# Performance work log

Measured on AMD Instinct MI355X. Metric: run time of the kernel, lower is better.

## Reference

```python
import jax, jax.numpy as jnp
import numpy as np

N_EMBD = 1024
N_HEAD = 16
HEAD_DIM = N_EMBD // N_HEAD
INNER = 4 * N_EMBD
EPS = 1e-5


def setup_inputs() -> dict:
    key = jax.random.key(0)
    ks = jax.random.split(key, 13)
    s = lambda d: 1.0 / np.sqrt(d)
    return {
        "x": jax.random.normal(ks[0], (2, 2048, N_EMBD), jnp.float32),
        "ln1_g": jnp.ones((N_EMBD,), jnp.float32),
        "ln1_b": jnp.zeros((N_EMBD,), jnp.float32),
        "w_attn": jax.random.normal(ks[1], (N_EMBD, 3 * N_EMBD), jnp.float32) * s(N_EMBD),
        "b_attn": jnp.zeros((3 * N_EMBD,), jnp.float32),
        "w_proj": jax.random.normal(ks[2], (N_EMBD, N_EMBD), jnp.float32) * s(N_EMBD),
        "b_proj": jnp.zeros((N_EMBD,), jnp.float32),
        "ln2_g": jnp.ones((N_EMBD,), jnp.float32),
        "ln2_b": jnp.zeros((N_EMBD,), jnp.float32),
        "w_fc": jax.random.normal(ks[3], (N_EMBD, INNER), jnp.float32) * s(N_EMBD),
        "b_fc": jnp.zeros((INNER,), jnp.float32),
        "w_fc2": jax.random.normal(ks[4], (INNER, N_EMBD), jnp.float32) * s(INNER),
        "b_fc2": jnpp if False else jnp.zeros((N_EMBD,), jnp.float32),
    }


def _layernorm(x, g, b):
    mu = jnp.mean(x, axis=-1, keepdims=True)
    var = jnp.mean(jnp.square(x - mu), axis=-1, keepdims=True)
    return (x - mu) * jax.lax.rsqrt(var + EPS) * g + b


def _attention(x, w_attn, b_attn, w_proj, b_proj):
    B, T, C = x.shape
    qkv = x @ w_attn + b_attn                      # [B,T,3C]
    q, k, v = jnp.split(qkv, 3, axis=-1)
    q = q.reshape(B, T, N_HEAD, HEAD_DIM).transpose(0, 2, 1, 3)  # [B,H,T,D]
    k = k.reshape(B, T, N_HEAD, HEAD_DIM).transpose(0, 2, 1, 3)
    v = v.reshape(B, T, N_HEAD, HEAD_DIM).transpose(0, 2, 1, 3)
    scale = HEAD_DIM ** -0.5
    scores = jnp.einsum("bhqd,bhkd->bhqk", q, k) * scale         # [B,H,T,T]
    causal = jnp.triu(jnp.ones((T, T), jnp.bool_), k=1)
    scores = jnp.where(causal, -jnp.inf, scores)
    attn = jax.nn.softmax(scores, axis=-1)
    out = jnp.einsum("bhqk,bhkd->bhqd", attn, v)                 # [B,H,T,D]
    out = out.transpose(0, 2, 1, 3).reshape(B, T, C)
    return out @ w_proj + b_proj


def reference(x, ln1_g, ln1_b, w_attn, b_attn, w_proj, b_proj,
              ln2_g, ln2_b, w_fc, b_fc, w_fc2, b_fc2):
    h = x + _attention(_layernorm(x, ln1_g, ln1_b), w_attn, b_attn, w_proj, b_proj)
    m = _layernorm(h, ln2_g, ln2_b)
    m = jax.nn.gelu(m @ w_fc + b_fc, approximate=False) @ w_fc2 + b_fc2
    return h + m
```

## Files before the change

### kernel.cpp

```cpp
#include <hip/hip_runtime.h>

typedef unsigned short u16;
typedef unsigned int u32;
typedef short v8s __attribute__((ext_vector_type(8)));
typedef short v4s __attribute__((ext_vector_type(4)));
typedef float v4f __attribute__((ext_vector_type(4)));

__device__ __forceinline__ float b2f(u16 v) {
    return __uint_as_float(((u32)v) << 16);
}
__device__ __forceinline__ u16 f2b(float f) {
    u32 u = __float_as_uint(f);
    return (u16)((u + 0x7FFFu + ((u >> 16) & 1u)) >> 16);
}

__device__ __forceinline__ void gload_lds16(const u16* g, u16* l) {
    __builtin_amdgcn_global_load_lds((const __attribute__((address_space(1))) void*)g,
                                     (__attribute__((address_space(3))) void*)l, 16, 0, 0);
}

__global__ void detect_k(const void* x, int* flag) {
    __shared__ int cnt;
    if (threadIdx.x == 0) cnt = 0;
    __syncthreads();
    const u16* p = (const u16*)x;
    int bad = 0;
    for (int i = threadIdx.x; i < 4096; i += 256) {
        int e = (p[i] >> 7) & 0xFF;
        if (e != 0 && (e < 100 || e > 140)) bad++;
    }
    atomicAdd(&cnt, bad);
    __syncthreads();
    if (threadIdx.x == 0) *flag = (cnt > 256) ? 1 : 0;
}

__global__ void cvt_k(const void* __restrict__ src, u16* __restrict__ dst, int n,
                      const int* __restrict__ flag) {
    const int isf32 = *flag;
    for (int i = blockIdx.x * 256 + threadIdx.x; i < n; i += gridDim.x * 256)
        dst[i] = isf32 ? f2b(((const float*)src)[i]) : ((const u16*)src)[i];
}

struct P8 { const void* p[8]; };
__global__ void cvt_small_k(P8 src, u16* __restrict__ bb, const int* __restrict__ flag) {
    const int isf32 = *flag;
    const int len[8] = {3072, 1024, 4096, 1024, 1024, 1024, 1024, 1024};
    const int doff[8] = {0, 4096, 8192, 12288, 16384, 17408, 18432, 19456};
    int gi = blockIdx.x * 256 + threadIdx.x;
    int seg = 0, off = gi;
    while (seg < 7 && off >= len[seg]) { off -= len[seg]; seg++; }
    if (off < len[seg]) {
        const void* s = src.p[seg];
        bb[doff[seg] + off] = isf32 ? f2b(((const float*)s)[off]) : ((const u16*)s)[off];
    }
}

__global__ void transpose_k(const void* __restrict__ in, u16* __restrict__ out, int R, int C,
                            const int* __restrict__ flag) {
    __shared__ u16 t[32][33];
    const int isf32 = *flag;
    const int c0 = blockIdx.x * 32, r0 = blockIdx.y * 32;
    for (int i = threadIdx.y; i < 32; i += 8) {
        size_t idx = (size_t)(r0 + i) * C + c0 + threadIdx.x;
        t[i][threadIdx.x] = isf32 ? f2b(((const float*)in)[idx]) : ((const u16*)in)[idx];
    }
    __syncthreads();
    for (int i = threadIdx.y; i < 32; i += 8)
        out[(size_t)(c0 + i) * R + r0 + threadIdx.x] = t[threadIdx.x][i];
}

__global__ __launch_bounds__(256) void layernorm_k(const u16* __restrict__ x,
                                                   const u16* __restrict__ g,
                                                   const u16* __restrict__ bta,
                                                   u16* __restrict__ out) {
    const int wid = threadIdx.x >> 6, lane = threadIdx.x & 63;
    const size_t row = (size_t)blockIdx.x * 4 + wid;
    const u16* xr = x + row * 1024 + lane * 16;
    u16 v[16];
    *(uint4*)&v[0] = *(const uint4*)xr;
    *(uint4*)&v[8] = *(const uint4*)(xr + 8);
    float f[16], s = 0.f, sq = 0.f;
#pragma unroll
    for (int i = 0; i < 16; i++) { f[i] = b2f(v[i]); s += f[i]; sq += f[i] * f[i]; }
#pragma unroll
    for (int d = 1; d < 64; d <<= 1) { s += __shfl_xor(s, d, 64); sq += __shfl_xor(sq, d, 64); }
    const float mean = s * (1.f / 1024.f);
    const float var = sq * (1.f / 1024.f) - mean * mean;
    const float rstd = rsqrtf(var + 1e-5f);
    u16 gv[16], bv[16];
    *(uint4*)&gv[0] = *(const uint4*)(g + lane * 16);
    *(uint4*)&gv[8] = *(const uint4*)(g + lane * 16 + 8);
    *(uint4*)&bv[0] = *(const uint4*)(bta + lane * 16);
    *(uint4*)&bv[8] = *(const uint4*)(bta + lane * 16 + 8);
    u16 ov[16];
#pragma unroll
    for (int i = 0; i < 16; i++) ov[i] = f2b((f[i] - mean) * rstd * b2f(gv[i]) + b2f(bv[i]));
    u16* orow = out + row * 1024 + lane * 16;
    *(uint4*)orow = *(uint4*)&ov[0];
    *(uint4*)(orow + 8) = *(uint4*)&ov[8];
}

#define GEMM_STAGE(tk, buf)                                              \
    do {                                                                 \
        const int _k = (tk) << 5;                                        \
        gload_lds16(Ag + _k, &As[buf][0] + wid * 512);                   \
        gload_lds16(Ag + (size_t)64 * K + _k, &As[buf][2048] + wid * 512); \
        gload_lds16(Bg + _k, &Bs[buf][0] + wid * 512);                   \
        gload_lds16(Bg + (size_t)64 * K + _k, &Bs[buf][2048] + wid * 512); \
    } while (0)

__global__ __launch_bounds__(256) void gemm_bt_k(const u16* __restrict__ A,
                                                 const u16* __restrict__ Bt,
                                                 const u16* __restrict__ bias,
                                                 const u16* __restrict__ res,
                                                 void* __restrict__ C,
                                                 int M, int N, int K, int do_gelu,
                                                 const int* __restrict__ outf32) {
    __shared__ __align__(16) u16 As[3][4096];
    __shared__ __align__(16) u16 Bs[3][4096];
    const int tid = threadIdx.x;
    const int wid = tid >> 6, lane = tid & 63;
    const int lg = lane >> 4, lm = lane & 15;
    const int wr = wid >> 1, wc = wid & 1;
    const int nwg = gridDim.x * gridDim.y;
    const int orig = blockIdx.y * gridDim.x + blockIdx.x;
    const int wg = (orig & 7) * (nwg >> 3) + (orig >> 3);
    const int m0 = (wg / gridDim.x) * 128, n0 = (wg % gridDim.x) * 128;

    const v4f vzero = {0.f, 0.f, 0.f, 0.f};
    v4f acc[4][4];
#pragma unroll
    for (int i = 0; i < 4; i++)
#pragma unroll
        for (int j = 0; j < 4; j++) acc[i][j] = vzero;

    const int srow = tid >> 2;
    const int scol = (((tid & 3) ^ ((tid >> 3) & 3)) * 8);
    const u16* Ag = A + (size_t)(m0 + srow) * K + scol;
    const u16* Bg = Bt + (size_t)(n0 + srow) * K + scol;
    const int lgx = (lg ^ ((lm >> 1) & 3)) * 8;

    const int nt = K >> 5;
    GEMM_STAGE(0, 0);
    GEMM_STAGE(1, 1);
    for (int t = 0; t < nt; ++t) {
        const int cur = t % 3;
        if (t + 2 < nt) {
            GEMM_STAGE(t + 2, (t + 2) % 3);
            asm volatile("s_waitcnt vmcnt(8)" ::: "memory");
        } else if (t + 1 < nt) {
            asm volatile("s_waitcnt vmcnt(4)" ::: "memory");
        } else {
            asm volatile("s_waitcnt vmcnt(0)" ::: "memory");
        }
        __builtin_amdgcn_s_barrier();
        v8s af[4], bf[4];
#pragma unroll
        for (int i = 0; i < 4; i++)
            af[i] = *(const v8s*)&As[cur][(wr * 64 + i * 16 + lm) * 32 + lgx];
#pragma unroll
        for (int j = 0; j < 4; j++)
            bf[j] = *(const v8s*)&Bs[cur][(wc * 64 + j * 16 + lm) * 32 + lgx];
        __builtin_amdgcn_s_setprio(1);
#pragma unroll
        for (int i = 0; i < 4; i++)
#pragma unroll
            for (int j = 0; j < 4; j++)
                acc[i][j] = __builtin_amdgcn_mfma_f32_16x16x32_bf16(af[i], bf[j], acc[i][j], 0, 0, 0);
        __builtin_amdgcn_s_setprio(0);
        asm volatile("s_waitcnt lgkmcnt(0)" ::: "memory");
        __builtin_amdgcn_sched_barrier(0);
        __builtin_amdgcn_s_barrier();
    }

    const int of32 = outf32 ? *outf32 : 0;
#pragma unroll
    for (int i = 0; i < 4; i++) {
#pragma unroll
        for (int r = 0; r < 4; r++) {
            const int row = m0 + wr * 64 + i * 16 + lg * 4 + r;
            const size_t rb = (size_t)row * N;
#pragma unroll
            for (int j = 0; j < 4; j++) {
                const int col = n0 + wc * 64 + j * 16 + lm;
                float v = acc[i][j][r] + b2f(bias[col]);
                if (do_gelu) v = 0.5f * v * (1.0f + erff(v * 0.70710678118f));
                if (res) v += b2f(res[rb + col]);
                if (of32) ((float*)C)[rb + col] = v;
                else ((u16*)C)[rb + col] = f2b(v);
            }
        }
    }
}

__global__ __launch_bounds__(256) void gemm_qkv_k(const u16* __restrict__ A,
                                                  const u16* __restrict__ Bt,
                                                  const u16* __restrict__ bias,
                                                  u16* __restrict__ Qh,
                                                  u16* __restrict__ Kh,
                                                  u16* __restrict__ Vth) {
    __shared__ __align__(16) u16 As[3][4096];
    __shared__ __align__(16) u16 Bs[3][4096];
    const int tid = threadIdx.x;
    const int wid = tid >> 6, lane = tid & 63;
    const int lg = lane >> 4, lm = lane & 15;
    const int wr = wid >> 1, wc = wid & 1;
    const int nwg = gridDim.x * gridDim.y;
    const int orig = blockIdx.y * gridDim.x + blockIdx.x;
    const int wg = (orig & 7) * (nwg >> 3) + (orig >> 3);
    const int m0 = (wg / gridDim.x) * 128, n0 = (wg % gridDim.x) * 128;
    const int K = 1024;

    const v4f vzero = {0.f, 0.f, 0.f, 0.f};
    v4f acc[4][4];
#pragma unroll
    for (int i = 0; i < 4; i++)
#pragma unroll
        for (int j = 0; j < 4; j++) acc[i][j] = vzero;

    const int srow = tid >> 2;
    const int scol = (((tid & 3) ^ ((tid >> 3) & 3)) * 8);
    const u16* Ag = A + (size_t)(m0 + srow) * K + scol;
    const u16* Bg = Bt + (size_t)(n0 + srow) * K + scol;
    const int lgx = (lg ^ ((lm >> 1) & 3)) * 8;

    const int nt = K >> 5;
    GEMM_STAGE(0, 0);
    GEMM_STAGE(1, 1);
    for (int t = 0; t < nt; ++t) {
        const int cur = t % 3;
        if (t + 2 < nt) {
            GEMM_STAGE(t + 2, (t + 2) % 3);
            asm volatile("s_waitcnt vmcnt(8)" ::: "memory");
        } else if (t + 1 < nt) {
            asm volatile("s_waitcnt vmcnt(4)" ::: "memory");
        } else {
            asm volatile("s_waitcnt vmcnt(0)" ::: "memory");
        }
        __builtin_amdgcn_s_barrier();
        v8s af[4], bf[4];
#pragma unroll
        for (int i = 0; i < 4; i++)
            af[i] = *(const v8s*)&As[cur][(wr * 64 + i * 16 + lm) * 32 + lgx];
#pragma unroll
        for (int j = 0; j < 4; j++)
            bf[j] = *(const v8s*)&Bs[cur][(wc * 64 + j * 16 + lm) * 32 + lgx];
        __builtin_amdgcn_s_setprio(1);
#pragma unroll
        for (int i = 0; i < 4; i++)
#pragma unroll
            for (int j = 0; j < 4; j++)
                acc[i][j] = __builtin_amdgcn_mfma_f32_16x16x32_bf16(af[i], bf[j], acc[i][j], 0, 0, 0);
        __builtin_amdgcn_s_setprio(0);
        asm volatile("s_waitcnt lgkmcnt(0)" ::: "memory");
        __builtin_amdgcn_sched_barrier(0);
        __builtin_amdgcn_s_barrier();
    }

    const int which = n0 >> 10;
    const int h = ((n0 & 1023) >> 6) + wc;
    if (which < 2) {
        u16* dst = which ? Kh : Qh;
        const float qsc = which ? 1.0f : 0.18033688011f;
#pragma unroll
        for (int i = 0; i < 4; i++) {
#pragma unroll
            for (int r = 0; r < 4; r++) {
                const int row = m0 + wr * 64 + i * 16 + lg * 4 + r;
                const int b = row >> 11, t = row & 2047;
                const size_t rb = ((size_t)(b * 16 + h) * 2048 + t) * 64;
#pragma unroll
                for (int j = 0; j < 4; j++) {
                    float v = (acc[i][j][r] + b2f(bias[n0 + wc * 64 + j * 16 + lm])) * qsc;
                    dst[rb + j * 16 + lm] = f2b(v);
                }
            }
        }
    } else {
#pragma unroll
        for (int i = 0; i < 4; i++) {
            const int t0 = m0 + wr * 64 + i * 16 + lg * 4;
            const int b = t0 >> 11, tt = t0 & 2047;
            const int w = tt & 31;
            const int pos = (tt & ~31) + ((w & 15) >> 2) * 8 + ((w >> 4) & 1) * 4;
#pragma unroll
            for (int j = 0; j < 4; j++) {
                const int d = j * 16 + lm;
                const float bv_ = b2f(bias[n0 + wc * 64 + j * 16 + lm]);
                u16 pk[4];
#pragma unroll
                for (int r = 0; r < 4; r++) pk[r] = f2b(acc[i][j][r] + bv_);
                *(v4s*)&Vth[((size_t)(b * 16 + h) * 64 + d) * 2048 + pos] = *(const v4s*)pk;
            }
        }
    }
}

__global__ __launch_bounds__(256, 4) void attn10_k(const u16* __restrict__ Qh,
                                                   const u16* __restrict__ Kh,
                                                   const u16* __restrict__ Vth,
                                                   u16* __restrict__ out) {
    __shared__ __align__(16) u16 Ks[2][4096];
    __shared__ __align__(16) u16 Vs[2][4096];
    const int tid = threadIdx.x;
    const int wid = tid >> 6, lane = tid & 63;
    const int lg = lane >> 4, lm = lane & 15;
    const int i = blockIdx.x;
    const int q = i >> 8, s = i & 255;
    const int bh = s & 31;
    const int g8 = s >> 5;
    const int g = (q == 0) ? g8 : (q == 1) ? (15 - g8) : (q == 2) ? (16 + g8) : (31 - g8);
    const int q0 = g * 64 + wid * 16;
    const int qrow_l = q0 + lm;
    const size_t qkb = (size_t)bh * 2048;
    const v4f vzero = {0.f, 0.f, 0.f, 0.f};
    const int nch = g + 1;

    const int r0 = tid >> 3;
    const int colp = ((tid & 7) * 16) ^ ((r0 & 7) << 4);
    const u16* Ksrc0 = Kh + (qkb + r0) * 64 + (colp >> 1);
    const u16* Ksrc1 = Ksrc0 + 32 * 64;
    const u16* Vsrc0 = Vth + ((size_t)bh * 64 + r0) * 2048 + (colp >> 1);
    const u16* Vsrc1 = Vsrc0 + (size_t)32 * 2048;
    const int wslot = wid * 512;

    const int xorv = (lm & 7) << 4;
    const int ro1 = (lm * 128 + ((lg * 16) ^ xorv)) >> 1;
    const int ro2 = (lm * 128 + (((lg * 16) + 64) ^ xorv)) >> 1;

    v8s aq[2];
    {
        const u16* qp = Qh + (qkb + q0 + lm) * 64 + lg * 8;
        aq[0] = *(const v8s*)qp;
        aq[1] = *(const v8s*)(qp + 32);
    }
    float l_run = 0.f;
    v4f o[4];
#pragma unroll
    for (int dt = 0; dt < 4; dt++) o[dt] = vzero;

    gload_lds16(Ksrc0, &Ks[0][0] + wslot);
    gload_lds16(Ksrc1, &Ks[0][2048] + wslot);
    gload_lds16(Vsrc0, &Vs[0][0] + wslot);
    gload_lds16(Vsrc1, &Vs[0][2048] + wslot);

    for (int ci = 0; ci < nch; ++ci) {
        const int cur = ci & 1;
        if (ci + 1 < nch) {
            const u16* kc = Ksrc0 + (ci + 1) * 4096;
            const u16* vc = Vsrc0 + (ci + 1) * 64;
            gload_lds16(kc, &Ks[cur ^ 1][0] + wslot);
            gload_lds16(kc + 32 * 64, &Ks[cur ^ 1][2048] + wslot);
            gload_lds16(vc, &Vs[cur ^ 1][0] + wslot);
            gload_lds16(vc + (size_t)32 * 2048, &Vs[cur ^ 1][2048] + wslot);
            asm volatile("s_waitcnt vmcnt(4)" ::: "memory");
        } else {
            asm volatile("s_waitcnt vmcnt(0)" ::: "memory");
        }
        __builtin_amdgcn_s_barrier();

        const u16* KB = &Ks[cur][0];
        const u16* VB = &Vs[cur][0];
        const int k0 = ci << 6;
        v4f sacc[4];
        __builtin_amdgcn_s_setprio(1);
#pragma unroll
        for (int kt = 0; kt < 4; kt++) {
            v8s klo = *(const v8s*)(KB + kt * 1024 + ro1);
            v8s khi = *(const v8s*)(KB + kt * 1024 + ro2);
            sacc[kt] = __builtin_amdgcn_mfma_f32_16x16x32_bf16(klo, aq[0], vzero, 0, 0, 0);
            sacc[kt] = __builtin_amdgcn_mfma_f32_16x16x32_bf16(khi, aq[1], sacc[kt], 0, 0, 0);
        }
        __builtin_amdgcn_s_setprio(0);
        float p[16];
        if (ci == nch - 1) {
#pragma unroll
            for (int kt = 0; kt < 4; kt++)
#pragma unroll
                for (int r = 0; r < 4; r++) {
                    float v = sacc[kt][r];
                    v = (k0 + kt * 16 + lg * 4 + r > qrow_l) ? -200.f : v;
                    p[kt * 4 + r] = exp2f(v);
                }
        } else {
#pragma unroll
            for (int kt = 0; kt < 4; kt++)
#pragma unroll
                for (int r = 0; r < 4; r++) p[kt * 4 + r] = exp2f(sacc[kt][r]);
        }
        float ls = 0.f;
#pragma unroll
        for (int e = 0; e < 16; e++) ls += p[e];
        l_run += ls;
        u32 pk[8];
#pragma unroll
        for (int j = 0; j < 8; j++) {
            u32 lo = __float_as_uint(p[j * 2]) + 0x8000u;
            u32 hi = __float_as_uint(p[j * 2 + 1]) + 0x8000u;
            pk[j] = __builtin_amdgcn_perm(hi, lo, 0x07060302u);
        }
        v8s B0, B1;
        ((u32*)&B0)[0] = pk[0]; ((u32*)&B0)[1] = pk[1];
        ((u32*)&B0)[2] = pk[2]; ((u32*)&B0)[3] = pk[3];
        ((u32*)&B1)[0] = pk[4]; ((u32*)&B1)[1] = pk[5];
        ((u32*)&B1)[2] = pk[6]; ((u32*)&B1)[3] = pk[7];
        __builtin_amdgcn_s_setprio(1);
#pragma unroll
        for (int dt = 0; dt < 4; dt++) {
            v8s vlo = *(const v8s*)(VB + dt * 1024 + ro1);
            v8s vhi = *(const v8s*)(VB + dt * 1024 + ro2);
            o[dt] = __builtin_amdgcn_mfma_f32_16x16x32_bf16(vlo, B0, o[dt], 0, 0, 0);
            o[dt] = __builtin_amdgcn_mfma_f32_16x16x32_bf16(vhi, B1, o[dt], 0, 0, 0);
        }
        __builtin_amdgcn_s_setprio(0);
        asm volatile("s_waitcnt lgkmcnt(0)" ::: "memory");
        __builtin_amdgcn_sched_barrier(0);
        __builtin_amdgcn_s_barrier();
    }
    l_run += __shfl_xor(l_run, 16, 64);
    l_run += __shfl_xor(l_run, 32, 64);
    const int b = bh >> 4, h = bh & 15;
    const float inv = 1.0f / l_run;
    const size_t rowb = ((size_t)b * 2048 + q0 + lm) * 1024 + h * 64;
#pragma unroll
    for (int dt = 0; dt < 4; dt++) {
        u16 pk2[4];
#pragma unroll
        for (int r = 0; r < 4; r++) pk2[r] = f2b(o[dt][r] * inv);
        *(v4s*)&out[rowb + dt * 16 + lg * 4] = *(const v4s*)pk2;
    }
}

extern "C" void kernel_launch(void* const* d_in, const int* in_sizes, int n_in,
                              void* d_out, int out_size, void* d_ws, size_t ws_size,
                              hipStream_t stream) {
    const void* x      = d_in[0];
    const void* ln1_g  = d_in[1];
    const void* ln1_b  = d_in[2];
    const void* w_attn = d_in[3];
    const void* b_attn = d_in[4];
    const void* w_proj = d_in[5];
    const void* b_proj = d_in[6];
    const void* ln2_g  = d_in[7];
    const void* ln2_b  = d_in[8];
    const void* w_fc   = d_in[9];
    const void* b_fc   = d_in[10];
    const void* w_fc2  = d_in[11];
    const void* b_fc2  = d_in[12];

    u16* ws = (u16*)d_ws;
    const size_t Mi = 1u << 20;
    u16* xb       = ws;
    u16* ln_buf   = ws + 4 * Mi;
    u16* h_buf    = ws + 8 * Mi;
    u16* wT_attn  = ws + 12 * Mi;
    u16* wT_proj  = ws + 15 * Mi;
    u16* wT_fc    = ws + 16 * Mi;
    u16* wT_fc2   = ws + 20 * Mi;
    u16* bb       = ws + 24 * Mi;
    u16* bb_attn = bb, *bb_proj = bb + 4096, *bb_fc = bb + 8192, *bb_fc2 = bb + 12288;
    u16* gsmall   = bb + 16384;
    u16* g_ln1g = gsmall, *g_ln1b = gsmall + 1024, *g_ln2g = gsmall + 2048, *g_ln2b = gsmall + 3072;
    int* flag     = (int*)(bb + 24576);
    u16* Qh       = ws + 25 * Mi;
    u16* Kh       = ws + 29 * Mi;
    u16* Vth      = ws + 33 * Mi;
    u16* attn_buf = ws + 37 * Mi;
    u16* fc_buf   = ws + 25 * Mi;

    detect_k<<<1, 256, 0, stream>>>(x, flag);

    cvt_k<<<4096, 256, 0, stream>>>(x, xb, 4 * Mi, flag);
    P8 smalls;
    smalls.p[0] = b_attn; smalls.p[1] = b_proj; smalls.p[2] = b_fc; smalls.p[3] = b_fc2;
    smalls.p[4] = ln1_g;  smalls.p[5] = ln1_b;  smalls.p[6] = ln2_g; smalls.p[7] = ln2_b;
    cvt_small_k<<<52, 256, 0, stream>>>(smalls, bb, flag);

    dim3 tb(32, 8);
    transpose_k<<<dim3(96, 32), tb, 0, stream>>>(w_attn, wT_attn, 1024, 3072, flag);
    transpose_k<<<dim3(32, 32), tb, 0, stream>>>(w_proj, wT_proj, 1024, 1024, flag);
    transpose_k<<<dim3(128, 32), tb, 0, stream>>>(w_fc, wT_fc, 1024, 4096, flag);
    transpose_k<<<dim3(32, 128), tb, 0, stream>>>(w_fc2, wT_fc2, 4096, 1024, flag);

    layernorm_k<<<1024, 256, 0, stream>>>(xb, g_ln1g, g_ln1b, ln_buf);
    gemm_qkv_k<<<dim3(24, 32), 256, 0, stream>>>(ln_buf, wT_attn, bb_attn, Qh, Kh, Vth);
    attn10_k<<<1024, 256, 0, stream>>>(Qh, Kh, Vth, attn_buf);
    gemm_bt_k<<<dim3(8, 32), 256, 0, stream>>>(attn_buf, wT_proj, bb_proj, xb, h_buf,
                                               4096, 1024, 1024, 0, nullptr);
    layernorm_k<<<1024, 256, 0, stream>>>(h_buf, g_ln2g, g_ln2b, ln_buf);
    gemm_bt_k<<<dim3(32, 32), 256, 0, stream>>>(ln_buf, wT_fc, bb_fc, nullptr, fc_buf,
                                                4096, 4096, 1024, 1, nullptr);
    gemm_bt_k<<<dim3(8, 32), 256, 0, stream>>>(fc_buf, wT_fc2, bb_fc2, h_buf, d_out,
                                               4096, 1024, 4096, 0, flag);
}
```

Baseline: 455.2 us.

## Add 256x256-tile 8-wave GEMM kernel for the FC1 GELU layer

```diff
diff --git a/kernel.cpp b/kernel.cpp
--- a/kernel.cpp
+++ b/kernel.cpp
@@ -12,6 +12,9 @@
 __device__ __forceinline__ u16 f2b(float f) {
     u32 u = __float_as_uint(f);
     return (u16)((u + 0x7FFFu + ((u >> 16) & 1u)) >> 16);
+}
+__device__ __forceinline__ v4f mfma16(v8s a, v8s b, v4f c) {
+    return __builtin_amdgcn_mfma_f32_16x16x32_bf16(a, b, c, 0, 0, 0);
 }
 
 __device__ __forceinline__ void gload_lds16(const u16* g, u16* l) {
@@ -183,6 +186,142 @@
 #pragma unroll
             for (int j = 0; j < 4; j++) {
                 const int col = n0 + wc * 64 + j * 16 + lm;
+                float v = acc[i][j][r] + b2f(bias[col]);
+                if (do_gelu) v = 0.5f * v * (1.0f + erff(v * 0.70710678118f));
+                if (res) v += b2f(res[rb + col]);
+                if (of32) ((float*)C)[rb + col] = v;
+                else ((u16*)C)[rb + col] = f2b(v);
+            }
+        }
+    }
+}
+
+#define ST256(LDSARR, P, tt, h)                                                  \
+    do {                                                                         \
+        const u16* _s = (P) + (size_t)((h) * 128) * K + (size_t)(tt) * 64;       \
+        gload_lds16(_s, &LDSARR[(tt) & 1][h][0] + wv * 512);                     \
+        gload_lds16(_s + (size_t)64 * K, &LDSARR[(tt) & 1][h][4096] + wv * 512); \
+    } while (0)
+
+#define MMROW(ii, x0, x1)                                   \
+    acc[ii][0] = mfma16(x0, bfr[0][0], acc[ii][0]);         \
+    acc[ii][0] = mfma16(x1, bfr[0][1], acc[ii][0]);         \
+    acc[ii][1] = mfma16(x0, bfr[1][0], acc[ii][1]);         \
+    acc[ii][1] = mfma16(x1, bfr[1][1], acc[ii][1]);         \
+    acc[ii][2] = mfma16(x0, bfr[2][0], acc[ii][2]);         \
+    acc[ii][2] = mfma16(x1, bfr[2][1], acc[ii][2]);         \
+    acc[ii][3] = mfma16(x0, bfr[3][0], acc[ii][3]);         \
+    acc[ii][3] = mfma16(x1, bfr[3][1], acc[ii][3]);
+
+#define RD_A2(i0, i1)                                         \
+    x0 = *(const v8s*)(ABase + (i0) * 1024 + offk0);          \
+    x1 = *(const v8s*)(ABase + (i0) * 1024 + offk1);          \
+    y0 = *(const v8s*)(ABase + (i1) * 1024 + offk0);          \
+    y1 = *(const v8s*)(ABase + (i1) * 1024 + offk1);
+
+__global__ __launch_bounds__(512, 2) void gemm256_k(const u16* __restrict__ A,
+                                                    const u16* __restrict__ Bt,
+                                                    const u16* __restrict__ bias,
+                                                    const u16* __restrict__ res,
+                                                    void* __restrict__ C,
+                                                    int M, int N, int K, int do_gelu,
+                                                    const int* __restrict__ outf32) {
+    __shared__ __align__(16) u16 As[2][2][8192];
+    __shared__ __align__(16) u16 Bs[2][2][8192];
+    const int tid = threadIdx.x;
+    const int wv = tid >> 6, lane = tid & 63;
+    const int lg = lane >> 4, lm = lane & 15;
+    const int wm = wv >> 2, wn = wv & 3;
+    const int nwg = gridDim.x * gridDim.y;
+    const int orig = blockIdx.y * gridDim.x + blockIdx.x;
+    const int wg = (orig & 7) * (nwg >> 3) + (orig >> 3);
+    const int m0 = (wg / gridDim.x) * 256, n0 = (wg % gridDim.x) * 256;
+
+    const v4f vzero = {0.f, 0.f, 0.f, 0.f};
+    v4f acc[8][4];
+#pragma unroll
+    for (int i = 0; i < 8; i++)
+#pragma unroll
+        for (int j = 0; j < 4; j++) acc[i][j] = vzero;
+
+    const int trow = tid >> 3;
+    const int csw = ((tid & 7) ^ (trow & 7)) * 8;
+    const u16* Ap = A + (size_t)(m0 + trow) * K + csw;
+    const u16* Bp = Bt + (size_t)(n0 + trow) * K + csw;
+    const int offk0 = lm * 64 + ((lg ^ (lm & 7)) << 3);
+    const int offk1 = offk0 ^ 32;
+
+    const int NT = K >> 6;
+    ST256(As, Ap, 0, 0); ST256(As, Ap, 0, 1);
+    ST256(Bs, Bp, 0, 0); ST256(Bs, Bp, 0, 1);
+    ST256(Bs, Bp, 1, 0); ST256(Bs, Bp, 1, 1);
+    asm volatile("s_waitcnt vmcnt(4)" ::: "memory");
+    __builtin_amdgcn_s_barrier();
+
+    for (int t = 0; t < NT; ++t) {
+        const int d = t & 1;
+        const u16* ABase = &As[d][wm][0];
+        const u16* BBase = &Bs[d][wn >> 1][(wn & 1) * 4096];
+        v8s bfr[4][2];
+        v8s x0, x1, y0, y1;
+#pragma unroll
+        for (int j = 0; j < 4; j++) {
+            bfr[j][0] = *(const v8s*)(BBase + j * 1024 + offk0);
+            bfr[j][1] = *(const v8s*)(BBase + j * 1024 + offk1);
+        }
+        RD_A2(0, 1)
+        if (t + 1 < NT) { ST256(As, Ap, t + 1, 0); }
+        __builtin_amdgcn_s_barrier();
+        asm volatile("s_waitcnt lgkmcnt(0)" ::: "memory");
+        __builtin_amdgcn_s_setprio(1);
+        MMROW(0, x0, x1)
+        MMROW(1, y0, y1)
+        __builtin_amdgcn_s_setprio(0);
+        __builtin_amdgcn_s_barrier();
+        RD_A2(2, 3)
+        if (t + 1 < NT) { ST256(As, Ap, t + 1, 1); }
+        __builtin_amdgcn_s_barrier();
+        asm volatile("s_waitcnt lgkmcnt(0)" ::: "memory");
+        __builtin_amdgcn_s_setprio(1);
+        MMROW(2, x0, x1)
+        MMROW(3, y0, y1)
+        __builtin_amdgcn_s_setprio(0);
+        __builtin_amdgcn_s_barrier();
+        RD_A2(4, 5)
+        if (t + 2 < NT) { ST256(Bs, Bp, t + 2, 0); }
+        __builtin_amdgcn_s_barrier();
+        asm volatile("s_waitcnt lgkmcnt(0)" ::: "memory");
+        __builtin_amdgcn_s_setprio(1);
+        MMROW(4, x0, x1)
+        MMROW(5, y0, y1)
+        __builtin_amdgcn_s_setprio(0);
+        __builtin_amdgcn_s_barrier();
+        RD_A2(6, 7)
+        if (t + 2 < NT) {
+            ST256(Bs, Bp, t + 2, 1);
+            asm volatile("s_waitcnt vmcnt(4)" ::: "memory");
+        } else {
+            asm volatile("s_waitcnt vmcnt(0)" ::: "memory");
+        }
+        __builtin_amdgcn_s_barrier();
+        asm volatile("s_waitcnt lgkmcnt(0)" ::: "memory");
+        __builtin_amdgcn_s_setprio(1);
+        MMROW(6, x0, x1)
+        MMROW(7, y0, y1)
+        __builtin_amdgcn_s_setprio(0);
+        __builtin_amdgcn_s_barrier();
+    }
+
+    const int of32 = outf32 ? *outf32 : 0;
+#pragma unroll
+    for (int i = 0; i < 8; i++) {
+#pragma unroll
+        for (int r = 0; r < 4; r++) {
+            const int row = m0 + wm * 128 + i * 16 + lg * 4 + r;
+            const size_t rb = (size_t)row * N;
+#pragma unroll
+            for (int j = 0; j < 4; j++) {
+                const int col = n0 + wn * 64 + j * 16 + lm;
                 float v = acc[i][j][r] + b2f(bias[col]);
                 if (do_gelu) v = 0.5f * v * (1.0f + erff(v * 0.70710678118f));
                 if (res) v += b2f(res[rb + col]);
@@ -488,7 +627,7 @@
     gemm_bt_k<<<dim3(8, 32), 256, 0, stream>>>(attn_buf, wT_proj, bb_proj, xb, h_buf,
                                                4096, 1024, 1024, 0, nullptr);
     layernorm_k<<<1024, 256, 0, stream>>>(h_buf, g_ln2g, g_ln2b, ln_buf);
-    gemm_bt_k<<<dim3(32, 32), 256, 0, stream>>>(ln_buf, wT_fc, bb_fc, nullptr, fc_buf,
+    gemm256_k<<<dim3(16, 16), 512, 0, stream>>>(ln_buf, wT_fc, bb_fc, nullptr, fc_buf,
                                                 4096, 4096, 1024, 1, nullptr);
     gemm_bt_k<<<dim3(8, 32), 256, 0, stream>>>(fc_buf, wT_fc2, bb_fc2, h_buf, d_out,
                                                4096, 1024, 4096, 0, flag);
```

Result: no change. 455.1 us (-0.0%).
